# Kernel tuning notes

Measured on AMD Instinct MI355X. Metric: run time of the kernel, lower is better.

## Reference

```python
import jax, jax.numpy as jnp
import numpy as np

B, F, H, E, O = 512, 512, 512, 8, 512  # batch, feature, hidden, experts, out_frame


def setup_inputs() -> dict:
    key = jax.random.key(0)
    ks = jax.random.split(key, 14)
    u = lambda k, shape, s: jax.random.uniform(k, shape, jnp.float32) * s
    return {
        "x": jax.random.normal(ks[0], (B, F), jnp.float32),
        # gating MLP params (torch Linear: y = x @ W.T + b)
        "gw0": u(ks[1], (H, F), 0.04) - 0.02,
        "gb0": jnp.zeros((H,), jnp.float32),
        "gw1": u(ks[2], (H, H), 0.04) - 0.02,
        "gb1": jnp.zeros((H,), jnp.float32),
        "gw2": u(ks[3], (E, H), 0.04) - 0.02,
        "gb2": jnp.zeros((E,), jnp.float32),
        # expert weight/bias banks
        "alpha0": u(ks[4], (E, H, F), 0.01),
        "beta0": jnp.zeros((E, H, 1), jnp.float32),
        "alpha1": u(ks[5], (E, H, H), 0.01),
        "beta1": jnp.zeros((E, H, 1), jnp.float32),
        "alpha2": u(ks[6], (E, O, H), 0.01),
        "beta2": jnp.zeros((E, O, 1), jnp.float32),
    }


def reference(x, gw0, gb0, gw1, gb1, gw2, gb2,
              alpha0, beta0, alpha1, beta1, alpha2, beta2):
    # gating network
    h = jax.nn.elu(x @ gw0.T + gb0)
    h = jax.nn.elu(h @ gw1.T + gb1)
    g = jax.nn.softmax(h @ gw2.T + gb2, axis=1)  # [B, E]

    # per-sample blended weights (sum over experts of gate-scaled expert mats)
    blend_w = lambda a: jnp.einsum('be,ehf->bhf', g, a)
    blend_b = lambda b: jnp.einsum('be,eh->bh', g, b[..., 0])

    # per-sample 3-layer MLP (bmm with vector rhs == batched matvec)
    H1 = jax.nn.elu(jnp.einsum('bhf,bf->bh', blend_w(alpha0), x) + blend_b(beta0))
    H2 = jax.nn.elu(jnp.einsum('bhf,bf->bh', blend_w(alpha1), H1) + blend_b(beta1))
    H3 = jnp.einsum('bof,bf->bo', blend_w(alpha2), H2) + blend_b(beta2)
    return H3
```

## Files before the change

kernel.cpp:

```cpp
#include <hip/hip_runtime.h>
#include <hip/hip_bf16.h>
#include <math.h>

enum { Bq = 512, Fq = 512, Hq = 512, Eq = 8, Oq = 512 };

typedef __attribute__((ext_vector_type(8))) short short8;
typedef __attribute__((ext_vector_type(4))) float floatx4;

static __device__ __forceinline__ unsigned short f2bf(float f) {
  unsigned u = __float_as_uint(f);
  u += 0x7fffu + ((u >> 16) & 1u);
  return (unsigned short)(u >> 16);
}
static __device__ __forceinline__ float bf2f(unsigned short h) {
  return __uint_as_float(((unsigned)h) << 16);
}
static __device__ __forceinline__ float elu1(float v) {
  return v > 0.f ? v : (__expf(v) - 1.f);
}

typedef __attribute__((address_space(1))) const unsigned int gu32;
typedef __attribute__((address_space(3))) unsigned int lu32;
static __device__ __forceinline__ void gld16(const unsigned short* g,
                                             unsigned short* l) {
  __builtin_amdgcn_global_load_lds((gu32*)g, (lu32*)l, 16, 0, 0);
}

static __device__ __forceinline__ int swz(int q, int r) {
  return (q & ~7) | ((q ^ r) & 7);
}

__global__ __launch_bounds__(256) void cvt6_kernel(
    const float* __restrict__ b0, const float* __restrict__ b1,
    const float* __restrict__ b2, unsigned short* __restrict__ db0,
    unsigned short* __restrict__ db1, unsigned short* __restrict__ db2,
    const float* __restrict__ s0, const float* __restrict__ s1,
    const float* __restrict__ s2, unsigned short* __restrict__ ds0,
    unsigned short* __restrict__ ds1, unsigned short* __restrict__ ds2,
    int nb, int ns) {
  int i = blockIdx.x * 256 + threadIdx.x;
  const float4* s;
  unsigned short* d;
  int j;
  if (i < 3 * nb) {
    int seg = i / nb;
    j = i - seg * nb;
    s = (seg == 0) ? (const float4*)b0
      : (seg == 1) ? (const float4*)b1 : (const float4*)b2;
    d = (seg == 0) ? db0 : (seg == 1) ? db1 : db2;
  } else {
    int k = i - 3 * nb;
    if (k >= 3 * ns) return;
    int seg = k / ns;
    j = k - seg * ns;
    s = (seg == 0) ? (const float4*)s0
      : (seg == 1) ? (const float4*)s1 : (const float4*)s2;
    d = (seg == 0) ? ds0 : (seg == 1) ? ds1 : ds2;
  }
  float4 v = s[j];
  ushort4 o;
  o.x = f2bf(v.x); o.y = f2bf(v.y); o.z = f2bf(v.z); o.w = f2bf(v.w);
  *(ushort4*)(d + 4 * (size_t)j) = o;
}

__global__ __launch_bounds__(256) void gating_gemm(
    const unsigned short* __restrict__ A, const unsigned short* __restrict__ W,
    const float* __restrict__ bias, unsigned short* __restrict__ C) {
  __shared__ unsigned short As[32 * 512];
  __shared__ unsigned short Ws[32 * 512];
  const int tid = threadIdx.x;
  const int wave = tid >> 6, lane = tid & 63;
  const int wm = wave >> 1, wn = wave & 1;
  const int lr = lane & 15, lk = lane >> 4;
  const int m0 = blockIdx.y * 32, n0 = blockIdx.x * 32;
#pragma unroll
  for (int i = 0; i < 8; i++) {
    int c = tid + i * 256;
    int r = c >> 6, ql = c & 63;
    gld16(&A[(size_t)(m0 + r) * 512 + swz(ql, r) * 8], &As[(c & ~63) * 8]);
  }
#pragma unroll
  for (int i = 0; i < 8; i++) {
    int c = tid + i * 256;
    int r = c >> 6, ql = c & 63;
    gld16(&W[(size_t)(n0 + r) * 512 + swz(ql, r) * 8], &Ws[(c & ~63) * 8]);
  }
  __syncthreads();
  const int rA = wm * 16 + lr, rB = wn * 16 + lr;
  floatx4 ac[4];
#pragma unroll
  for (int j = 0; j < 4; j++) ac[j] = (floatx4){0.f, 0.f, 0.f, 0.f};
#pragma unroll
  for (int t = 0; t < 4; t++) {
#pragma unroll
    for (int j = 0; j < 4; j++) {
      int q = ((j * 128 + t * 32) >> 3) + lk;
      short8 av = *(const short8*)&As[rA * 512 + swz(q, rA) * 8];
      short8 bv = *(const short8*)&Ws[rB * 512 + swz(q, rB) * 8];
      ac[j] = __builtin_amdgcn_mfma_f32_16x16x32_bf16(av, bv, ac[j], 0, 0, 0);
    }
  }
  floatx4 acc = (ac[0] + ac[1]) + (ac[2] + ac[3]);
  int n = n0 + wn * 16 + lr;
  float bn = bias[n];
#pragma unroll
  for (int r = 0; r < 4; r++) {
    int m = m0 + wm * 16 + lk * 4 + r;
    C[(size_t)m * 512 + n] = f2bf(elu1(acc[r] + bn));
  }
}

__global__ __launch_bounds__(256) void expert_gemm(
    const unsigned short* __restrict__ A,
    const unsigned short* __restrict__ Wb,
    const float* __restrict__ g,
    float* __restrict__ P) {
  __shared__ unsigned short As[32 * 256];
  __shared__ unsigned short Ws[2][32 * 256];
  const int tid = threadIdx.x;
  const int wave = tid >> 6, lane = tid & 63;
  const int wm = wave >> 1, wn = wave & 1;
  const int lr = lane & 15, lk = lane >> 4;
  const int m0 = blockIdx.y * 32, n0 = blockIdx.x * 32;
  const int kz = blockIdx.z, kbeg = kz * 256;

#pragma unroll
  for (int i = 0; i < 4; i++) {
    int c = tid + i * 256;
    int r = c >> 5, ql = c & 31;
    gld16(&A[(size_t)(m0 + r) * 512 + kbeg + swz(ql, r) * 8],
          &As[(c & ~63) * 8]);
  }
#pragma unroll
  for (int i = 0; i < 4; i++) {
    int c = tid + i * 256;
    int r = c >> 5, ql = c & 31;
    gld16(&Wb[(size_t)(n0 + r) * 512 + kbeg + swz(ql, r) * 8],
          &Ws[0][(c & ~63) * 8]);
  }
  float g8[4][8];
#pragma unroll
  for (int r = 0; r < 4; r++) {
    int m = m0 + wm * 16 + lk * 4 + r;
    float4 ga = *(const float4*)&g[(size_t)m * 8];
    float4 gb = *(const float4*)&g[(size_t)m * 8 + 4];
    g8[r][0] = ga.x; g8[r][1] = ga.y; g8[r][2] = ga.z; g8[r][3] = ga.w;
    g8[r][4] = gb.x; g8[r][5] = gb.y; g8[r][6] = gb.z; g8[r][7] = gb.w;
  }

  const int rA = wm * 16 + lr, rB = wn * 16 + lr;
  floatx4 fin = {0.f, 0.f, 0.f, 0.f};
#pragma unroll
  for (int e = 0; e < 8; e++) {
    __syncthreads();
    if (e < 7) {
      const unsigned short* Wn = Wb + ((size_t)(e + 1) * 512 + n0) * 512 + kbeg;
#pragma unroll
      for (int i = 0; i < 4; i++) {
        int c = tid + i * 256;
        int r = c >> 5, ql = c & 31;
        gld16(&Wn[(size_t)r * 512 + swz(ql, r) * 8],
              &Ws[(e + 1) & 1][(c & ~63) * 8]);
      }
    }
    const unsigned short* wb = Ws[e & 1];
    floatx4 c0 = {0.f, 0.f, 0.f, 0.f}, c1 = {0.f, 0.f, 0.f, 0.f};
#pragma unroll
    for (int s = 0; s < 8; s++) {
      int q = s * 4 + lk;
      short8 av = *(const short8*)&As[rA * 256 + swz(q, rA) * 8];
      short8 bv = *(const short8*)&wb[rB * 256 + swz(q, rB) * 8];
      if (s & 1)
        c1 = __builtin_amdgcn_mfma_f32_16x16x32_bf16(av, bv, c1, 0, 0, 0);
      else
        c0 = __builtin_amdgcn_mfma_f32_16x16x32_bf16(av, bv, c0, 0, 0, 0);
    }
    floatx4 ae = c0 + c1;
#pragma unroll
    for (int r = 0; r < 4; r++) fin[r] += g8[r][e] * ae[r];
  }

  float* Po = P + (size_t)kz * Bq * Hq;
  int n = n0 + wn * 16 + lr;
#pragma unroll
  for (int r = 0; r < 4; r++) {
    int m = m0 + wm * 16 + lk * 4 + r;
    Po[(size_t)m * 512 + n] = fin[r];
  }
}

__global__ __launch_bounds__(64) void gate_kernel(
    const unsigned short* __restrict__ G1,
    const float* __restrict__ gw2,
    const float* __restrict__ gb2,
    float* __restrict__ g) {
  int b = blockIdx.x;
  int lane = threadIdx.x;
  float xv[8];
#pragma unroll
  for (int t = 0; t < 8; t++) xv[t] = bf2f(G1[(size_t)b * Hq + t * 64 + lane]);
  float le[Eq];
#pragma unroll
  for (int e = 0; e < Eq; e++) {
    float p = 0.f;
#pragma unroll
    for (int t = 0; t < 8; t++)
      p += xv[t] * gw2[(size_t)e * Hq + t * 64 + lane];
#pragma unroll
    for (int o = 32; o > 0; o >>= 1) p += __shfl_xor(p, o);
    le[e] = p + gb2[e];
  }
  float m = le[0];
#pragma unroll
  for (int e = 1; e < Eq; e++) m = fmaxf(m, le[e]);
  float s = 0.f;
#pragma unroll
  for (int e = 0; e < Eq; e++) {
    le[e] = __expf(le[e] - m);
    s += le[e];
  }
  float inv = 1.f / s;
  if (lane == 0) {
#pragma unroll
    for (int e = 0; e < Eq; e++) g[(size_t)b * Eq + e] = le[e] * inv;
  }
}

template <int ACT>
__global__ __launch_bounds__(256) void reduce_kernel(
    const float* __restrict__ P,
    const float* __restrict__ g,
    const float* __restrict__ beta,
    unsigned short* __restrict__ outb, float* __restrict__ outf) {
  int idx = blockIdx.x * 256 + threadIdx.x;
  int b = idx >> 7, h4 = (idx & 127) << 2;
  float4 v0 = *(const float4*)&P[((size_t)b) * Hq + h4];
  float4 v1 = *(const float4*)&P[((size_t)Bq + b) * Hq + h4];
  float4 s = {v0.x + v1.x, v0.y + v1.y, v0.z + v1.z, v0.w + v1.w};
  const float* gb = g + (size_t)b * Eq;
#pragma unroll
  for (int e = 0; e < Eq; e++) {
    float ge = gb[e];
    float4 bv = *(const float4*)&beta[e * Hq + h4];
    s.x += ge * bv.x; s.y += ge * bv.y; s.z += ge * bv.z; s.w += ge * bv.w;
  }
  if (ACT) {
    ushort4 o;
    o.x = f2bf(elu1(s.x)); o.y = f2bf(elu1(s.y));
    o.z = f2bf(elu1(s.z)); o.w = f2bf(elu1(s.w));
    *(ushort4*)&outb[(size_t)idx * 4] = o;
  } else {
    *(float4*)&outf[(size_t)idx * 4] = s;
  }
}

extern "C" void kernel_launch(void* const* d_in, const int* in_sizes, int n_in,
                              void* d_out, int out_size, void* d_ws,
                              size_t ws_size, hipStream_t stream) {
  const float* x = (const float*)d_in[0];
  const float* gw0 = (const float*)d_in[1];
  const float* gb0 = (const float*)d_in[2];
  const float* gw1 = (const float*)d_in[3];
  const float* gb1 = (const float*)d_in[4];
  const float* gw2 = (const float*)d_in[5];
  const float* gb2 = (const float*)d_in[6];
  const float* alpha0 = (const float*)d_in[7];
  const float* beta0 = (const float*)d_in[8];
  const float* alpha1 = (const float*)d_in[9];
  const float* beta1 = (const float*)d_in[10];
  const float* alpha2 = (const float*)d_in[11];
  const float* beta2 = (const float*)d_in[12];
  float* out = (float*)d_out;

  char* ws = (char*)d_ws;
  auto alloc = [&](size_t bytes) {
    char* p = ws;
    ws += (bytes + 255) & ~(size_t)255;
    return p;
  };
  unsigned short* xb = (unsigned short*)alloc((size_t)Bq * Fq * 2);
  unsigned short* gw0b = (unsigned short*)alloc((size_t)Hq * Fq * 2);
  unsigned short* gw1b = (unsigned short*)alloc((size_t)Hq * Hq * 2);
  unsigned short* a0b = (unsigned short*)alloc((size_t)Eq * Hq * Fq * 2);
  unsigned short* a1b = (unsigned short*)alloc((size_t)Eq * Hq * Hq * 2);
  unsigned short* a2b = (unsigned short*)alloc((size_t)Eq * Oq * Hq * 2);
  unsigned short* G0b = (unsigned short*)alloc((size_t)Bq * Hq * 2);
  unsigned short* G1b = (unsigned short*)alloc((size_t)Bq * Hq * 2);
  unsigned short* H1b = (unsigned short*)alloc((size_t)Bq * Hq * 2);
  unsigned short* H2b = (unsigned short*)alloc((size_t)Bq * Hq * 2);
  float* gates = (float*)alloc((size_t)Bq * Eq * 4);
  float* P = (float*)alloc((size_t)2 * Bq * Hq * 4);

  {
    int nb = (Eq * Hq * Fq) / 4, ns = (Bq * Fq) / 4;
    int total = 3 * nb + 3 * ns;
    cvt6_kernel<<<(total + 255) / 256, 256, 0, stream>>>(
        alpha0, alpha1, alpha2, a0b, a1b, a2b, x, gw0, gw1, xb, gw0b, gw1b,
        nb, ns);
  }

  dim3 gg(16, 16);
  gating_gemm<<<gg, 256, 0, stream>>>(xb, gw0b, gb0, G0b);
  gating_gemm<<<gg, 256, 0, stream>>>(G0b, gw1b, gb1, G1b);

  gate_kernel<<<Bq, 64, 0, stream>>>(G1b, gw2, gb2, gates);

  dim3 ge(16, 16, 2);
  dim3 gr((Bq * Hq / 4) / 256);
  expert_gemm<<<ge, 256, 0, stream>>>(xb, a0b, gates, P);
  reduce_kernel<1><<<gr, 256, 0, stream>>>(P, gates, beta0, H1b, nullptr);
  expert_gemm<<<ge, 256, 0, stream>>>(H1b, a1b, gates, P);
  reduce_kernel<1><<<gr, 256, 0, stream>>>(P, gates, beta1, H2b, nullptr);
  expert_gemm<<<ge, 256, 0, stream>>>(H2b, a2b, gates, P);
  reduce_kernel<0><<<gr, 256, 0, stream>>>(P, gates, beta2, nullptr, out);
}
```

Baseline: 139.7 us.

## Fuse split-K reduction, bias and ELU into the next expert GEMM's A-load

Moves the gate-weighted bias addition into the kz==0 epilogue of each expert GEMM. The next GEMM now reads both fp32 split-K partials, sums them, applies ELU and converts to bf16 while staging its A tile in shared memory. This drops two intermediate reduce launches and the bf16 H1/H2 round trips, leaving only a final sum kernel. In exchange, every N-column block re-reads the fp32 partials and recomputes ELU redundantly, and the A load becomes a synchronous register path instead of an async global-to-LDS copy.

```diff
diff --git a/kernel.cpp b/kernel.cpp
--- a/kernel.cpp
+++ b/kernel.cpp
@@ -110,11 +110,14 @@
   }
 }
 
+template <int FROMP>
 __global__ __launch_bounds__(256) void expert_gemm(
     const unsigned short* __restrict__ A,
+    const float* __restrict__ Pin,
     const unsigned short* __restrict__ Wb,
     const float* __restrict__ g,
-    float* __restrict__ P) {
+    const float* __restrict__ beta,
+    float* __restrict__ Pout) {
   __shared__ unsigned short As[32 * 256];
   __shared__ unsigned short Ws[2][32 * 256];
   const int tid = threadIdx.x;
@@ -124,12 +127,34 @@
   const int m0 = blockIdx.y * 32, n0 = blockIdx.x * 32;
   const int kz = blockIdx.z, kbeg = kz * 256;
 
-#pragma unroll
-  for (int i = 0; i < 4; i++) {
-    int c = tid + i * 256;
-    int r = c >> 5, ql = c & 31;
-    gld16(&A[(size_t)(m0 + r) * 512 + kbeg + swz(ql, r) * 8],
-          &As[(c & ~63) * 8]);
+  if (FROMP) {
+#pragma unroll
+    for (int i = 0; i < 4; i++) {
+      int c = tid + i * 256;
+      int r = c >> 5, q = c & 31;
+      const float* p0 = Pin + (size_t)(m0 + r) * 512 + kbeg + q * 8;
+      const float* p1 = p0 + (size_t)Bq * Hq;
+      float4 x0 = *(const float4*)p0, x1 = *(const float4*)(p0 + 4);
+      float4 y0 = *(const float4*)p1, y1 = *(const float4*)(p1 + 4);
+      short8 o;
+      o[0] = (short)f2bf(elu1(x0.x + y0.x));
+      o[1] = (short)f2bf(elu1(x0.y + y0.y));
+      o[2] = (short)f2bf(elu1(x0.z + y0.z));
+      o[3] = (short)f2bf(elu1(x0.w + y0.w));
+      o[4] = (short)f2bf(elu1(x1.x + y1.x));
+      o[5] = (short)f2bf(elu1(x1.y + y1.y));
+      o[6] = (short)f2bf(elu1(x1.z + y1.z));
+      o[7] = (short)f2bf(elu1(x1.w + y1.w));
+      *(short8*)&As[(r * 32 + swz(q, r)) * 8] = o;
+    }
+  } else {
+#pragma unroll
+    for (int i = 0; i < 4; i++) {
+      int c = tid + i * 256;
+      int r = c >> 5, ql = c & 31;
+      gld16(&A[(size_t)(m0 + r) * 512 + kbeg + swz(ql, r) * 8],
+            &As[(c & ~63) * 8]);
+    }
   }
 #pragma unroll
   for (int i = 0; i < 4; i++) {
@@ -180,8 +205,20 @@
     for (int r = 0; r < 4; r++) fin[r] += g8[r][e] * ae[r];
   }
 
-  float* Po = P + (size_t)kz * Bq * Hq;
   int n = n0 + wn * 16 + lr;
+  if (kz == 0) {
+    float bv[8];
+#pragma unroll
+    for (int e = 0; e < 8; e++) bv[e] = beta[e * 512 + n];
+#pragma unroll
+    for (int r = 0; r < 4; r++) {
+      float bs = 0.f;
+#pragma unroll
+      for (int e = 0; e < 8; e++) bs += g8[r][e] * bv[e];
+      fin[r] += bs;
+    }
+  }
+  float* Po = Pout + (size_t)kz * Bq * Hq;
 #pragma unroll
   for (int r = 0; r < 4; r++) {
     int m = m0 + wm * 16 + lk * 4 + r;
@@ -226,32 +263,13 @@
   }
 }
 
-template <int ACT>
-__global__ __launch_bounds__(256) void reduce_kernel(
-    const float* __restrict__ P,
-    const float* __restrict__ g,
-    const float* __restrict__ beta,
-    unsigned short* __restrict__ outb, float* __restrict__ outf) {
+__global__ __launch_bounds__(256) void reduce_final(
+    const float* __restrict__ P, float* __restrict__ outf) {
   int idx = blockIdx.x * 256 + threadIdx.x;
-  int b = idx >> 7, h4 = (idx & 127) << 2;
-  float4 v0 = *(const float4*)&P[((size_t)b) * Hq + h4];
-  float4 v1 = *(const float4*)&P[((size_t)Bq + b) * Hq + h4];
+  const float4 v0 = ((const float4*)P)[idx];
+  const float4 v1 = ((const float4*)(P + (size_t)Bq * Hq))[idx];
   float4 s = {v0.x + v1.x, v0.y + v1.y, v0.z + v1.z, v0.w + v1.w};
-  const float* gb = g + (size_t)b * Eq;
-#pragma unroll
-  for (int e = 0; e < Eq; e++) {
-    float ge = gb[e];
-    float4 bv = *(const float4*)&beta[e * Hq + h4];
-    s.x += ge * bv.x; s.y += ge * bv.y; s.z += ge * bv.z; s.w += ge * bv.w;
-  }
-  if (ACT) {
-    ushort4 o;
-    o.x = f2bf(elu1(s.x)); o.y = f2bf(elu1(s.y));
-    o.z = f2bf(elu1(s.z)); o.w = f2bf(elu1(s.w));
-    *(ushort4*)&outb[(size_t)idx * 4] = o;
-  } else {
-    *(float4*)&outf[(size_t)idx * 4] = s;
-  }
+  ((float4*)outf)[idx] = s;
 }
 
 extern "C" void kernel_launch(void* const* d_in, const int* in_sizes, int n_in,
@@ -286,10 +304,9 @@
   unsigned short* a2b = (unsigned short*)alloc((size_t)Eq * Oq * Hq * 2);
   unsigned short* G0b = (unsigned short*)alloc((size_t)Bq * Hq * 2);
   unsigned short* G1b = (unsigned short*)alloc((size_t)Bq * Hq * 2);
-  unsigned short* H1b = (unsigned short*)alloc((size_t)Bq * Hq * 2);
-  unsigned short* H2b = (unsigned short*)alloc((size_t)Bq * Hq * 2);
   float* gates = (float*)alloc((size_t)Bq * Eq * 4);
-  float* P = (float*)alloc((size_t)2 * Bq * Hq * 4);
+  float* P1 = (float*)alloc((size_t)2 * Bq * Hq * 4);
+  float* P2 = (float*)alloc((size_t)2 * Bq * Hq * 4);
 
   {
     int nb = (Eq * Hq * Fq) / 4, ns = (Bq * Fq) / 4;
@@ -306,11 +323,8 @@
   gate_kernel<<<Bq, 64, 0, stream>>>(G1b, gw2, gb2, gates);
 
   dim3 ge(16, 16, 2);
-  dim3 gr((Bq * Hq / 4) / 256);
-  expert_gemm<<<ge, 256, 0, stream>>>(xb, a0b, gates, P);
-  reduce_kernel<1><<<gr, 256, 0, stream>>>(P, gates, beta0, H1b, nullptr);
-  expert_gemm<<<ge, 256, 0, stream>>>(H1b, a1b, gates, P);
-  reduce_kernel<1><<<gr, 256, 0, stream>>>(P, gates, beta1, H2b, nullptr);
-  expert_gemm<<<ge, 256, 0, stream>>>(H2b, a2b, gates, P);
-  reduce_kernel<0><<<gr, 256, 0, stream>>>(P, gates, beta2, nullptr, out);
-}
+  expert_gemm<0><<<ge, 256, 0, stream>>>(xb, nullptr, a0b, gates, beta0, P1);
+  expert_gemm<1><<<ge, 256, 0, stream>>>(nullptr, P1, a1b, gates, beta1, P2);
+  expert_gemm<1><<<ge, 256, 0, stream>>>(nullptr, P2, a2b, gates, beta2, P1);
+  reduce_final<<<(Bq * Hq / 4) / 256, 256, 0, stream>>>(P1, out);
+}
```

After: 137.3 us. About the same (-1.7%).
